# Optimization experiments

Measured on AMD Instinct MI355X. Metric: run time of the kernel, lower is better.

## Reference

```python
import jax, jax.numpy as jnp
import numpy as np

DIM = 1024
NUM_HEADS = 16
HEAD_DIM = DIM // NUM_HEADS
B, L = 2, 2048


def setup_inputs() -> dict:
    key = jax.random.key(0)
    k_x, k_qkv, k_pw, k_pb = jax.random.split(key, 4)
    x = jax.random.normal(k_x, (B, L, DIM), dtype=jnp.float32)
    # nn.Linear(dim, 3*dim, bias=False): weight [3*dim, dim]; y = x @ W.T
    w_qkv = jax.random.normal(k_qkv, (3 * DIM, DIM), dtype=jnp.float32) * (DIM ** -0.5)
    # nn.Linear(dim, dim) with bias
    w_proj = jax.random.normal(k_pw, (DIM, DIM), dtype=jnp.float32) * (DIM ** -0.5)
    b_proj = jax.random.normal(k_pb, (DIM,), dtype=jnp.float32) * 0.01
    return {"x": x, "w_qkv": w_qkv, "w_proj": w_proj, "b_proj": b_proj}


def reference(x, w_qkv, w_proj, b_proj):
    Bx, Lx, C = x.shape
    qkv = x @ w_qkv.T  # [B, L, 3C]
    qkv = qkv.reshape(Bx, Lx, 3, NUM_HEADS, HEAD_DIM)
    q = jnp.transpose(qkv[:, :, 0], (0, 2, 1, 3))  # [B, H, L, D]
    k = jnp.transpose(qkv[:, :, 1], (0, 2, 1, 3))
    v = jnp.transpose(qkv[:, :, 2], (0, 2, 1, 3))
    attn = jnp.einsum('bhqd,bhkd->bhqk', q, k) * (HEAD_DIM ** -0.5)
    attn = jax.nn.softmax(attn, axis=-1)
    out = jnp.einsum('bhqk,bhkd->bhqd', attn, v)  # [B, H, L, D]
    out = jnp.transpose(out, (0, 2, 1, 3)).reshape(Bx, Lx, C)
    return out @ w_proj.T + b_proj
```

## Files before the change

### kernel.cpp

```cpp
#include <hip/hip_runtime.h>

#define DIM 1024
#define NH 16
#define HD 64
#define BB 2
#define LL 2048
#define BL (BB*LL)
#define NQKV (3*DIM)

typedef __bf16 bf16;
typedef __bf16 bf16x4 __attribute__((ext_vector_type(4)));
typedef __bf16 bf16x8 __attribute__((ext_vector_type(8)));
typedef float  f32x4  __attribute__((ext_vector_type(4)));

#define QSCALE 0.1803368801111204f

typedef __attribute__((address_space(3))) unsigned int lds_u32;
typedef __attribute__((address_space(1))) unsigned int glb_u32;

__device__ __forceinline__ void gld_lds16(const bf16* g, bf16* l) {
    __builtin_amdgcn_global_load_lds((const glb_u32*)g, (lds_u32*)l, 16, 0, 0);
}

#define C0 (BL*DIM/4)
#define C1 (NQKV*DIM/4)
#define C2 (DIM*DIM/4)
__global__ __launch_bounds__(256) void cvt_all(const float* __restrict__ x,
        const float* __restrict__ wq, const float* __restrict__ wp,
        bf16* __restrict__ xb, bf16* __restrict__ wqb, bf16* __restrict__ wpb) {
    int i = blockIdx.x * 256 + threadIdx.x;
    const float* in; bf16* out; int j;
    if (i < C0)            { in = x;  out = xb;  j = i; }
    else if (i < C0 + C1)  { in = wq; out = wqb; j = i - C0; }
    else                   { in = wp; out = wpb; j = i - C0 - C1; }
    float4 f = ((const float4*)in)[j];
    bf16x4 o = { (bf16)f.x, (bf16)f.y, (bf16)f.z, (bf16)f.w };
    ((bf16x4*)out)[j] = o;
}

__global__ __launch_bounds__(256, 3) void gemm_qkv(
        const bf16* __restrict__ A, const bf16* __restrict__ W,
        bf16* __restrict__ Qb, bf16* __restrict__ Kb, bf16* __restrict__ VTb) {
    __shared__ bf16 As[128][64];
    __shared__ bf16 Bs[128][64];
    const int tid = threadIdx.x;
    const int w = tid >> 6, lane = tid & 63, quad = lane >> 4, l16 = lane & 15;
    const int n0 = blockIdx.x * 128, m0 = blockIdx.y * 128;
    const int wm = (w & 1) * 64, wn = (w >> 1) * 64;
    f32x4 acc[4][4] = {};
    for (int k0 = 0; k0 < DIM; k0 += 64) {
        #pragma unroll
        for (int i = 0; i < 4; ++i) {
            int cb = w * 256 + i * 64;
            int gc = cb + lane;
            int r = gc >> 3;
            int cs = (gc & 7) ^ (r & 7);
            gld_lds16(A + (size_t)(m0 + r) * DIM + k0 + cs*8, &As[0][0] + cb * 8);
            gld_lds16(W + (size_t)(n0 + r) * DIM + k0 + cs*8, &Bs[0][0] + cb * 8);
        }
        __syncthreads();
        #pragma unroll
        for (int kc = 0; kc < 2; ++kc) {
            bf16x8 af[4], bfr[4];
            #pragma unroll
            for (int t = 0; t < 4; ++t) {
                int rw = wn + t*16 + l16;
                int cw = (kc*4 + quad) ^ (rw & 7);
                af[t] = *(const bf16x8*)(&Bs[0][0] + rw*64 + cw*8);
                int rx = wm + t*16 + l16;
                int cx = (kc*4 + quad) ^ (rx & 7);
                bfr[t] = *(const bf16x8*)(&As[0][0] + rx*64 + cx*8);
            }
            #pragma unroll
            for (int tm = 0; tm < 4; ++tm)
                #pragma unroll
                for (int tn = 0; tn < 4; ++tn)
                    acc[tm][tn] = __builtin_amdgcn_mfma_f32_16x16x32_bf16(
                                      af[tm], bfr[tn], acc[tm][tn], 0, 0, 0);
        }
        __syncthreads();
    }
    const int which = n0 >> 10;
    #pragma unroll
    for (int tm = 0; tm < 4; ++tm) {
        int nb = n0 + wn + tm*16 + quad*4;
        int rem = nb & 1023, h = rem >> 6, db = rem & 63;
        #pragma unroll
        for (int tn = 0; tn < 4; ++tn) {
            int m = m0 + wm + tn*16 + l16;
            int b = m >> 11, l = m & 2047, bh = (b << 4) | h;
            if (which == 0) {
                bf16x4 q4 = { (bf16)(acc[tm][tn][0] * QSCALE),
                              (bf16)(acc[tm][tn][1] * QSCALE),
                              (bf16)(acc[tm][tn][2] * QSCALE),
                              (bf16)(acc[tm][tn][3] * QSCALE) };
                *(bf16x4*)(Qb + ((size_t)bh << 17) + ((size_t)l << 6) + db) = q4;
            } else if (which == 1) {
                bf16x4 k4 = { (bf16)acc[tm][tn][0], (bf16)acc[tm][tn][1],
                              (bf16)acc[tm][tn][2], (bf16)acc[tm][tn][3] };
                *(bf16x4*)(Kb + ((size_t)bh << 17) + ((size_t)l << 6) + db) = k4;
            } else {
                #pragma unroll
                for (int r = 0; r < 4; ++r)
                    VTb[((size_t)bh << 17) + ((size_t)(db + r) << 11) + l] =
                        (bf16)acc[tm][tn][r];
            }
        }
    }
}

__global__ __launch_bounds__(256, 3) void gemm_proj(
        const bf16* __restrict__ A, const bf16* __restrict__ W,
        const float* __restrict__ bias, float* __restrict__ out) {
    __shared__ bf16 As[2][128][64];
    __shared__ bf16 Bs[2][64][64];
    const int tid = threadIdx.x;
    const int w = tid >> 6, lane = tid & 63, quad = lane >> 4, l16 = lane & 15;
    const int n0 = blockIdx.x * 64, m0 = blockIdx.y * 128;
    const int wm = (w & 1) * 64, wn = (w >> 1) * 32;
    f32x4 acc[2][4] = {};

    auto stage = [&](int k0, int buf) {
        #pragma unroll
        for (int i = 0; i < 4; ++i) {
            int cb = w * 256 + i * 64;
            int gc = cb + lane;
            int r = gc >> 3;
            int cs = (gc & 7) ^ (r & 7);
            gld_lds16(A + (size_t)(m0 + r) * DIM + k0 + cs*8,
                      &As[buf][0][0] + cb * 8);
        }
        #pragma unroll
        for (int i = 0; i < 2; ++i) {
            int cb = w * 128 + i * 64;
            int gc = cb + lane;
            int r = gc >> 3;
            int cs = (gc & 7) ^ (r & 7);
            gld_lds16(W + (size_t)(n0 + r) * DIM + k0 + cs*8,
                      &Bs[buf][0][0] + cb * 8);
        }
    };

    stage(0, 0);
    for (int ks = 0; ks < 16; ++ks) {
        const int cur = ks & 1;
        __syncthreads();
        if (ks < 15) stage((ks + 1) * 64, cur ^ 1);
        #pragma unroll
        for (int kc = 0; kc < 2; ++kc) {
            bf16x8 af[2], bfr[4];
            #pragma unroll
            for (int t = 0; t < 2; ++t) {
                int rw = wn + t*16 + l16;
                int cw = (kc*4 + quad) ^ (rw & 7);
                af[t] = *(const bf16x8*)(&Bs[cur][0][0] + rw*64 + cw*8);
            }
            #pragma unroll
            for (int t = 0; t < 4; ++t) {
                int rx = wm + t*16 + l16;
                int cx = (kc*4 + quad) ^ (rx & 7);
                bfr[t] = *(const bf16x8*)(&As[cur][0][0] + rx*64 + cx*8);
            }
            #pragma unroll
            for (int tm = 0; tm < 2; ++tm)
                #pragma unroll
                for (int tn = 0; tn < 4; ++tn)
                    acc[tm][tn] = __builtin_amdgcn_mfma_f32_16x16x32_bf16(
                                      af[tm], bfr[tn], acc[tm][tn], 0, 0, 0);
        }
    }
    #pragma unroll
    for (int tm = 0; tm < 2; ++tm) {
        int nb = n0 + wn + tm*16 + quad*4;
        float4 b4 = *(const float4*)&bias[nb];
        #pragma unroll
        for (int tn = 0; tn < 4; ++tn) {
            int m = m0 + wm + tn*16 + l16;
            float4 o4 = { acc[tm][tn][0] + b4.x, acc[tm][tn][1] + b4.y,
                          acc[tm][tn][2] + b4.z, acc[tm][tn][3] + b4.w };
            *(float4*)(out + (size_t)m * DIM + nb) = o4;
        }
    }
}

__global__ __launch_bounds__(512, 2) void attn(
        const bf16* __restrict__ Qb, const bf16* __restrict__ Kb,
        const bf16* __restrict__ VTb, bf16* __restrict__ AO) {
    __shared__ __align__(16) char smem[66048];
    bf16* KsP  = (bf16*)smem;
    bf16* VTsP = (bf16*)(smem + 32768);
    const int tid = threadIdx.x;
    const int w = tid >> 6, lane = tid & 63, quad = lane >> 4, l16 = lane & 15;
    const int qw = w & 3, kvh = w >> 2;
    const int linear = blockIdx.y * 8 + blockIdx.x;
    const int swz = (linear & 7) * 32 + (linear >> 3);
    const int qt = swz & 7, bh = swz >> 3;
    const bf16* Qg = Qb + ((size_t)bh << 17) + (size_t)(qt * 256) * 64;
    const bf16* Kg = Kb + ((size_t)bh << 17);
    const bf16* Vg = VTb + ((size_t)bh << 17);

    bf16x8 aq[4][2];
    #pragma unroll
    for (int sub = 0; sub < 4; ++sub)
        #pragma unroll
        for (int kd = 0; kd < 2; ++kd)
            aq[sub][kd] = *(const bf16x8*)(Qg + (size_t)(qw*64 + sub*16 + l16) * 64
                                           + kd*32 + quad*8);

    bf16x8 onesf = {};
    if (l16 == 0)
        #pragma unroll
        for (int j = 0; j < 8; ++j) onesf[j] = (bf16)1.0f;

    f32x4 oacc[4][4] = {};
    f32x4 lacc[4] = {};
    const f32x4 zero4 = {};
    bf16x8 ap[4][2];

    auto stageK = [&](int kt, int buf) {
        #pragma unroll
        for (int sub = 0; sub < 2; ++sub) {
            int r = tid >> 3;
            int cs = (tid & 7) ^ (r & 7) ^ ((r >> 3) & 7) ^ ((r & 1) << 2);
            gld_lds16(Kg + (size_t)(kt*128 + sub*64 + r) * 64 + cs*8,
                      KsP + (buf*2 + sub) * 4096 + tid*8);
        }
    };
    auto stageV = [&](int kt, int buf) {
        #pragma unroll
        for (int sub = 0; sub < 2; ++sub) {
            int r = tid >> 3;
            int cs = (tid & 7) ^ (r & 7) ^ ((r >> 3) & 7);
            gld_lds16(Vg + (size_t)r * 2048 + kt*128 + sub*64 + cs*8,
                      VTsP + (buf*2 + sub) * 4096 + tid*8);
        }
    };
    auto pv = [&](int pbuf) {
        __builtin_amdgcn_s_setprio(1);
        #pragma unroll
        for (int kk = 0; kk < 2; ++kk) {
            #pragma unroll
            for (int nt = 0; nt < 4; ++nt) {
                int row = nt*16 + l16;
                int cp = (kk*4 + quad) ^ (row & 7) ^ ((row >> 3) & 7);
                bf16x8 bv = *(const bf16x8*)(VTsP + (pbuf*2 + kvh) * 4096
                                             + row*64 + cp*8);
                #pragma unroll
                for (int sub = 0; sub < 4; ++sub)
                    oacc[sub][nt] = __builtin_amdgcn_mfma_f32_16x16x32_bf16(
                                        ap[sub][kk], bv, oacc[sub][nt], 0, 0, 0);
            }
            #pragma unroll
            for (int sub = 0; sub < 4; ++sub)
                lacc[sub] = __builtin_amdgcn_mfma_f32_16x16x32_bf16(
                                ap[sub][kk], onesf, lacc[sub], 0, 0, 0);
        }
        __builtin_amdgcn_s_setprio(0);
    };

    auto body = [&](int kt, int cur) {
        __syncthreads();
        if (kt < 15) stageK(kt + 1, cur ^ 1);
        stageV(kt, cur);

        if (kt > 0) pv(cur ^ 1);

        f32x4 s[4][2][2];
        __builtin_amdgcn_s_setprio(1);
        #pragma unroll
        for (int kk = 0; kk < 2; ++kk)
            #pragma unroll
            for (int u = 0; u < 2; ++u) {
                int rk = kk*32 + ((l16 >> 2) << 3) + u*4 + (l16 & 3);
                int f = (rk & 7) ^ ((rk >> 3) & 7) ^ ((rk & 1) << 2);
                const bf16* kb = KsP + (cur*2 + kvh) * 4096 + rk*64;
                bf16x8 kf0 = *(const bf16x8*)(kb + ((0*4 + quad) ^ f)*8);
                bf16x8 kf1 = *(const bf16x8*)(kb + ((1*4 + quad) ^ f)*8);
                #pragma unroll
                for (int sub = 0; sub < 4; ++sub) {
                    s[sub][kk][u] = __builtin_amdgcn_mfma_f32_16x16x32_bf16(
                                        kf0, aq[sub][0], zero4, 0, 0, 0);
                    s[sub][kk][u] = __builtin_amdgcn_mfma_f32_16x16x32_bf16(
                                        kf1, aq[sub][1], s[sub][kk][u], 0, 0, 0);
                }
            }
        __builtin_amdgcn_s_setprio(0);

        #pragma unroll
        for (int sub = 0; sub < 4; ++sub)
            #pragma unroll
            for (int kk = 0; kk < 2; ++kk) {
                bf16x8 p;
                #pragma unroll
                for (int u = 0; u < 2; ++u)
                    #pragma unroll
                    for (int r = 0; r < 4; ++r)
                        p[u*4 + r] = (bf16)__builtin_amdgcn_exp2f(s[sub][kk][u][r]);
                ap[sub][kk] = p;
            }
    };

    stageK(0, 0);
    for (int kt2 = 0; kt2 < 16; kt2 += 2) {
        body(kt2,     0);
        body(kt2 + 1, 1);
    }
    __syncthreads();
    pv(1);

    float* OredF = (float*)smem;
    float* LredF = (float*)(smem + 32768);
    const int b = bh >> 4, h = bh & 15;
    #pragma unroll
    for (int t = 0; t < 2; ++t) {
        __syncthreads();
        if (kvh == 1 && (qw >> 1) == t) {
            int slot = qw & 1;
            #pragma unroll
            for (int sub = 0; sub < 4; ++sub)
                #pragma unroll
                for (int nt = 0; nt < 4; ++nt)
                    #pragma unroll
                    for (int r = 0; r < 4; ++r)
                        OredF[((slot*4 + sub)*16 + quad*4 + r)*64 + nt*16 + l16]
                            = oacc[sub][nt][r];
            if (l16 == 0)
                #pragma unroll
                for (int sub = 0; sub < 4; ++sub)
                    #pragma unroll
                    for (int r = 0; r < 4; ++r)
                        LredF[(slot*4 + sub)*16 + quad*4 + r] = lacc[sub][r];
        }
        __syncthreads();
        if (kvh == 0 && (qw >> 1) == t) {
            int slot = qw & 1;
            #pragma unroll
            for (int sub = 0; sub < 4; ++sub)
                #pragma unroll
                for (int nt = 0; nt < 4; ++nt)
                    #pragma unroll
                    for (int r = 0; r < 4; ++r)
                        oacc[sub][nt][r] +=
                            OredF[((slot*4 + sub)*16 + quad*4 + r)*64 + nt*16 + l16];
            if (l16 == 0)
                #pragma unroll
                for (int sub = 0; sub < 4; ++sub)
                    #pragma unroll
                    for (int r = 0; r < 4; ++r)
                        lacc[sub][r] += LredF[(slot*4 + sub)*16 + quad*4 + r];
            #pragma unroll
            for (int sub = 0; sub < 4; ++sub)
                #pragma unroll
                for (int r = 0; r < 4; ++r) {
                    float l = __shfl(lacc[sub][r], quad * 16, 64);
                    float inv = 1.0f / l;
                    int lq = qt*256 + qw*64 + sub*16 + quad*4 + r;
                    size_t rowbase = ((size_t)(b * 2048 + lq)) * DIM + h * 64;
                    #pragma unroll
                    for (int nt = 0; nt < 4; ++nt)
                        AO[rowbase + nt*16 + l16] = (bf16)(oacc[sub][nt][r] * inv);
                }
        }
    }
}

extern "C" void kernel_launch(void* const* d_in, const int* in_sizes, int n_in,
                              void* d_out, int out_size, void* d_ws, size_t ws_size,
                              hipStream_t stream) {
    const float* x      = (const float*)d_in[0];
    const float* w_qkv  = (const float*)d_in[1];
    const float* w_proj = (const float*)d_in[2];
    const float* b_proj = (const float*)d_in[3];
    float* out = (float*)d_out;
    char* ws = (char*)d_ws;

    bf16* xb  = (bf16*)(ws);
    bf16* wqb = (bf16*)(ws + ( 8u << 20));
    bf16* wpb = (bf16*)(ws + (14u << 20));
    bf16* Qb  = (bf16*)(ws + (16u << 20));
    bf16* Kb  = (bf16*)(ws + (24u << 20));
    bf16* VTb = (bf16*)(ws + (32u << 20));
    bf16* AOb = (bf16*)(ws + (40u << 20));

    cvt_all<<<(C0 + C1 + C2) / 256, 256, 0, stream>>>(x, w_qkv, w_proj, xb, wqb, wpb);
    gemm_qkv<<<dim3(NQKV/128, BL/128), 256, 0, stream>>>(xb, wqb, Qb, Kb, VTb);
    attn<<<dim3(LL/256, BB*NH),        512, 0, stream>>>(Qb, Kb, VTb, AOb);
    gemm_proj<<<dim3(DIM/64, BL/128),  256, 0, stream>>>(AOb, wpb, b_proj, out);
}
```

Measured before the change: 166.5 us.

## Enlarge proj GEMM tile to 128x128 and drop double buffering

```diff
diff --git a/kernel.cpp b/kernel.cpp
--- a/kernel.cpp
+++ b/kernel.cpp
@@ -112,65 +112,47 @@
 __global__ __launch_bounds__(256, 3) void gemm_proj(
         const bf16* __restrict__ A, const bf16* __restrict__ W,
         const float* __restrict__ bias, float* __restrict__ out) {
-    __shared__ bf16 As[2][128][64];
-    __shared__ bf16 Bs[2][64][64];
+    __shared__ bf16 As[128][64];
+    __shared__ bf16 Bs[128][64];
     const int tid = threadIdx.x;
     const int w = tid >> 6, lane = tid & 63, quad = lane >> 4, l16 = lane & 15;
-    const int n0 = blockIdx.x * 64, m0 = blockIdx.y * 128;
-    const int wm = (w & 1) * 64, wn = (w >> 1) * 32;
-    f32x4 acc[2][4] = {};
-
-    auto stage = [&](int k0, int buf) {
+    const int n0 = blockIdx.x * 128, m0 = blockIdx.y * 128;
+    const int wm = (w & 1) * 64, wn = (w >> 1) * 64;
+    f32x4 acc[4][4] = {};
+    for (int k0 = 0; k0 < DIM; k0 += 64) {
         #pragma unroll
         for (int i = 0; i < 4; ++i) {
             int cb = w * 256 + i * 64;
             int gc = cb + lane;
             int r = gc >> 3;
             int cs = (gc & 7) ^ (r & 7);
-            gld_lds16(A + (size_t)(m0 + r) * DIM + k0 + cs*8,
-                      &As[buf][0][0] + cb * 8);
-        }
-        #pragma unroll
-        for (int i = 0; i < 2; ++i) {
-            int cb = w * 128 + i * 64;
-            int gc = cb + lane;
-            int r = gc >> 3;
-            int cs = (gc & 7) ^ (r & 7);
-            gld_lds16(W + (size_t)(n0 + r) * DIM + k0 + cs*8,
-                      &Bs[buf][0][0] + cb * 8);
-        }
-    };
-
-    stage(0, 0);
-    for (int ks = 0; ks < 16; ++ks) {
-        const int cur = ks & 1;
-        __syncthreads();
-        if (ks < 15) stage((ks + 1) * 64, cur ^ 1);
+            gld_lds16(A + (size_t)(m0 + r) * DIM + k0 + cs*8, &As[0][0] + cb * 8);
+            gld_lds16(W + (size_t)(n0 + r) * DIM + k0 + cs*8, &Bs[0][0] + cb * 8);
+        }
+        __syncthreads();
         #pragma unroll
         for (int kc = 0; kc < 2; ++kc) {
-            bf16x8 af[2], bfr[4];
-            #pragma unroll
-            for (int t = 0; t < 2; ++t) {
+            bf16x8 af[4], bfr[4];
+            #pragma unroll
+            for (int t = 0; t < 4; ++t) {
                 int rw = wn + t*16 + l16;
                 int cw = (kc*4 + quad) ^ (rw & 7);
-                af[t] = *(const bf16x8*)(&Bs[cur][0][0] + rw*64 + cw*8);
-            }
-            #pragma unroll
-            for (int t = 0; t < 4; ++t) {
+                af[t] = *(const bf16x8*)(&Bs[0][0] + rw*64 + cw*8);
                 int rx = wm + t*16 + l16;
                 int cx = (kc*4 + quad) ^ (rx & 7);
-                bfr[t] = *(const bf16x8*)(&As[cur][0][0] + rx*64 + cx*8);
-            }
-            #pragma unroll
-            for (int tm = 0; tm < 2; ++tm)
+                bfr[t] = *(const bf16x8*)(&As[0][0] + rx*64 + cx*8);
+            }
+            #pragma unroll
+            for (int tm = 0; tm < 4; ++tm)
                 #pragma unroll
                 for (int tn = 0; tn < 4; ++tn)
                     acc[tm][tn] = __builtin_amdgcn_mfma_f32_16x16x32_bf16(
                                       af[tm], bfr[tn], acc[tm][tn], 0, 0, 0);
         }
+        __syncthreads();
     }
     #pragma unroll
-    for (int tm = 0; tm < 2; ++tm) {
+    for (int tm = 0; tm < 4; ++tm) {
         int nb = n0 + wn + tm*16 + quad*4;
         float4 b4 = *(const float4*)&bias[nb];
         #pragma unroll
@@ -385,5 +367,5 @@
     cvt_all<<<(C0 + C1 + C2) / 256, 256, 0, stream>>>(x, w_qkv, w_proj, xb, wqb, wpb);
     gemm_qkv<<<dim3(NQKV/128, BL/128), 256, 0, stream>>>(xb, wqb, Qb, Kb, VTb);
     attn<<<dim3(LL/256, BB*NH),        512, 0, stream>>>(Qb, Kb, VTb, AOb);
-    gemm_proj<<<dim3(DIM/64, BL/128),  256, 0, stream>>>(AOb, wpb, b_proj, out);
-}
+    gemm_proj<<<dim3(DIM/128, BL/128), 256, 0, stream>>>(AOb, wpb, b_proj, out);
+}
```

After: 176.4 us. 1.06x slower.

## Split attention KV tile across four wave groups with 1024-thread blocks

Applied to the files above, without the earlier changes.

```diff
diff --git a/kernel.cpp b/kernel.cpp
--- a/kernel.cpp
+++ b/kernel.cpp
@@ -183,10 +183,10 @@
     }
 }
 
-__global__ __launch_bounds__(512, 2) void attn(
+__global__ __launch_bounds__(1024, 4) void attn(
         const bf16* __restrict__ Qb, const bf16* __restrict__ Kb,
         const bf16* __restrict__ VTb, bf16* __restrict__ AO) {
-    __shared__ __align__(16) char smem[66048];
+    __shared__ __align__(16) char smem[66560];
     bf16* KsP  = (bf16*)smem;
     bf16* VTsP = (bf16*)(smem + 32768);
     const int tid = threadIdx.x;
@@ -215,46 +215,39 @@
     f32x4 oacc[4][4] = {};
     f32x4 lacc[4] = {};
     const f32x4 zero4 = {};
-    bf16x8 ap[4][2];
+    bf16x8 ap[4];
 
     auto stageK = [&](int kt, int buf) {
-        #pragma unroll
-        for (int sub = 0; sub < 2; ++sub) {
-            int r = tid >> 3;
-            int cs = (tid & 7) ^ (r & 7) ^ ((r >> 3) & 7) ^ ((r & 1) << 2);
-            gld_lds16(Kg + (size_t)(kt*128 + sub*64 + r) * 64 + cs*8,
-                      KsP + (buf*2 + sub) * 4096 + tid*8);
-        }
+        int sub = tid >> 9, tl = tid & 511;
+        int r = tl >> 3;
+        int cs = (tl & 7) ^ (r & 7) ^ ((r >> 3) & 7) ^ ((r & 1) << 2);
+        gld_lds16(Kg + (size_t)(kt*128 + sub*64 + r) * 64 + cs*8,
+                  KsP + (buf*2 + sub) * 4096 + tl*8);
     };
     auto stageV = [&](int kt, int buf) {
-        #pragma unroll
-        for (int sub = 0; sub < 2; ++sub) {
-            int r = tid >> 3;
-            int cs = (tid & 7) ^ (r & 7) ^ ((r >> 3) & 7);
-            gld_lds16(Vg + (size_t)r * 2048 + kt*128 + sub*64 + cs*8,
-                      VTsP + (buf*2 + sub) * 4096 + tid*8);
-        }
+        int sub = tid >> 9, tl = tid & 511;
+        int r = tl >> 3;
+        int cs = (tl & 7) ^ (r & 7) ^ ((r >> 3) & 7);
+        gld_lds16(Vg + (size_t)r * 2048 + kt*128 + sub*64 + cs*8,
+                  VTsP + (buf*2 + sub) * 4096 + tl*8);
     };
     auto pv = [&](int pbuf) {
         __builtin_amdgcn_s_setprio(1);
         #pragma unroll
-        for (int kk = 0; kk < 2; ++kk) {
-            #pragma unroll
-            for (int nt = 0; nt < 4; ++nt) {
-                int row = nt*16 + l16;
-                int cp = (kk*4 + quad) ^ (row & 7) ^ ((row >> 3) & 7);
-                bf16x8 bv = *(const bf16x8*)(VTsP + (pbuf*2 + kvh) * 4096
-                                             + row*64 + cp*8);
-                #pragma unroll
-                for (int sub = 0; sub < 4; ++sub)
-                    oacc[sub][nt] = __builtin_amdgcn_mfma_f32_16x16x32_bf16(
-                                        ap[sub][kk], bv, oacc[sub][nt], 0, 0, 0);
-            }
-            #pragma unroll
-            for (int sub = 0; sub < 4; ++sub)
-                lacc[sub] = __builtin_amdgcn_mfma_f32_16x16x32_bf16(
-                                ap[sub][kk], onesf, lacc[sub], 0, 0, 0);
-        }
+        for (int nt = 0; nt < 4; ++nt) {
+            int row = nt*16 + l16;
+            int cp = ((kvh & 1)*4 + quad) ^ (row & 7) ^ ((row >> 3) & 7);
+            bf16x8 bv = *(const bf16x8*)(VTsP + (pbuf*2 + (kvh >> 1)) * 4096
+                                         + row*64 + cp*8);
+            #pragma unroll
+            for (int sub = 0; sub < 4; ++sub)
+                oacc[sub][nt] = __builtin_amdgcn_mfma_f32_16x16x32_bf16(
+                                    ap[sub], bv, oacc[sub][nt], 0, 0, 0);
+        }
+        #pragma unroll
+        for (int sub = 0; sub < 4; ++sub)
+            lacc[sub] = __builtin_amdgcn_mfma_f32_16x16x32_bf16(
+                            ap[sub], onesf, lacc[sub], 0, 0, 0);
         __builtin_amdgcn_s_setprio(0);
     };
 
@@ -265,39 +258,35 @@
 
         if (kt > 0) pv(cur ^ 1);
 
-        f32x4 s[4][2][2];
+        f32x4 s[4][2];
         __builtin_amdgcn_s_setprio(1);
         #pragma unroll
-        for (int kk = 0; kk < 2; ++kk)
-            #pragma unroll
-            for (int u = 0; u < 2; ++u) {
-                int rk = kk*32 + ((l16 >> 2) << 3) + u*4 + (l16 & 3);
-                int f = (rk & 7) ^ ((rk >> 3) & 7) ^ ((rk & 1) << 2);
-                const bf16* kb = KsP + (cur*2 + kvh) * 4096 + rk*64;
-                bf16x8 kf0 = *(const bf16x8*)(kb + ((0*4 + quad) ^ f)*8);
-                bf16x8 kf1 = *(const bf16x8*)(kb + ((1*4 + quad) ^ f)*8);
-                #pragma unroll
-                for (int sub = 0; sub < 4; ++sub) {
-                    s[sub][kk][u] = __builtin_amdgcn_mfma_f32_16x16x32_bf16(
-                                        kf0, aq[sub][0], zero4, 0, 0, 0);
-                    s[sub][kk][u] = __builtin_amdgcn_mfma_f32_16x16x32_bf16(
-                                        kf1, aq[sub][1], s[sub][kk][u], 0, 0, 0);
-                }
+        for (int u = 0; u < 2; ++u) {
+            int rk = (kvh & 1)*32 + ((l16 >> 2) << 3) + u*4 + (l16 & 3);
+            int f = (rk & 7) ^ ((rk >> 3) & 7) ^ ((rk & 1) << 2);
+            const bf16* kb = KsP + (cur*2 + (kvh >> 1)) * 4096 + rk*64;
+            bf16x8 kf0 = *(const bf16x8*)(kb + ((0*4 + quad) ^ f)*8);
+            bf16x8 kf1 = *(const bf16x8*)(kb + ((1*4 + quad) ^ f)*8);
+            #pragma unroll
+            for (int sub = 0; sub < 4; ++sub) {
+                s[sub][u] = __builtin_amdgcn_mfma_f32_16x16x32_bf16(
+                                kf0, aq[sub][0], zero4, 0, 0, 0);
+                s[sub][u] = __builtin_amdgcn_mfma_f32_16x16x32_bf16(
+                                kf1, aq[sub][1], s[sub][u], 0, 0, 0);
             }
+        }
         __builtin_amdgcn_s_setprio(0);
 
         #pragma unroll
-        for (int sub = 0; sub < 4; ++sub)
-            #pragma unroll
-            for (int kk = 0; kk < 2; ++kk) {
-                bf16x8 p;
-                #pragma unroll
-                for (int u = 0; u < 2; ++u)
-                    #pragma unroll
-                    for (int r = 0; r < 4; ++r)
-                        p[u*4 + r] = (bf16)__builtin_amdgcn_exp2f(s[sub][kk][u][r]);
-                ap[sub][kk] = p;
-            }
+        for (int sub = 0; sub < 4; ++sub) {
+            bf16x8 p;
+            #pragma unroll
+            for (int u = 0; u < 2; ++u)
+                #pragma unroll
+                for (int r = 0; r < 4; ++r)
+                    p[u*4 + r] = (bf16)__builtin_amdgcn_exp2f(s[sub][u][r]);
+            ap[sub] = p;
+        }
     };
 
     stageK(0, 0);
@@ -309,13 +298,14 @@
     pv(1);
 
     float* OredF = (float*)smem;
-    float* LredF = (float*)(smem + 32768);
+    float* LredF = (float*)(smem + 65536);
     const int b = bh >> 4, h = bh & 15;
     #pragma unroll
     for (int t = 0; t < 2; ++t) {
-        __syncthreads();
-        if (kvh == 1 && (qw >> 1) == t) {
-            int slot = qw & 1;
+        const bool grp = (qw >> 1) == t;
+        __syncthreads();
+        if (grp && (kvh & 1)) {
+            int slot = (qw & 1)*2 + (kvh >> 1);
             #pragma unroll
             for (int sub = 0; sub < 4; ++sub)
                 #pragma unroll
@@ -332,8 +322,44 @@
                         LredF[(slot*4 + sub)*16 + quad*4 + r] = lacc[sub][r];
         }
         __syncthreads();
-        if (kvh == 0 && (qw >> 1) == t) {
-            int slot = qw & 1;
+        if (grp && !(kvh & 1)) {
+            int slot = (qw & 1)*2 + (kvh >> 1);
+            #pragma unroll
+            for (int sub = 0; sub < 4; ++sub)
+                #pragma unroll
+                for (int nt = 0; nt < 4; ++nt)
+                    #pragma unroll
+                    for (int r = 0; r < 4; ++r)
+                        oacc[sub][nt][r] +=
+                            OredF[((slot*4 + sub)*16 + quad*4 + r)*64 + nt*16 + l16];
+            if (l16 == 0)
+                #pragma unroll
+                for (int sub = 0; sub < 4; ++sub)
+                    #pragma unroll
+                    for (int r = 0; r < 4; ++r)
+                        lacc[sub][r] += LredF[(slot*4 + sub)*16 + quad*4 + r];
+        }
+        __syncthreads();
+        if (grp && kvh == 2) {
+            int slot = (qw & 1)*2;
+            #pragma unroll
+            for (int sub = 0; sub < 4; ++sub)
+                #pragma unroll
+                for (int nt = 0; nt < 4; ++nt)
+                    #pragma unroll
+                    for (int r = 0; r < 4; ++r)
+                        OredF[((slot*4 + sub)*16 + quad*4 + r)*64 + nt*16 + l16]
+                            = oacc[sub][nt][r];
+            if (l16 == 0)
+                #pragma unroll
+                for (int sub = 0; sub < 4; ++sub)
+                    #pragma unroll
+                    for (int r = 0; r < 4; ++r)
+                        LredF[(slot*4 + sub)*16 + quad*4 + r] = lacc[sub][r];
+        }
+        __syncthreads();
+        if (grp && kvh == 0) {
+            int slot = (qw & 1)*2;
             #pragma unroll
             for (int sub = 0; sub < 4; ++sub)
                 #pragma unroll
@@ -384,6 +410,6 @@
 
     cvt_all<<<(C0 + C1 + C2) / 256, 256, 0, stream>>>(x, w_qkv, w_proj, xb, wqb, wpb);
     gemm_qkv<<<dim3(NQKV/128, BL/128), 256, 0, stream>>>(xb, wqb, Qb, Kb, VTb);
-    attn<<<dim3(LL/256, BB*NH),        512, 0, stream>>>(Qb, Kb, VTb, AOb);
+    attn<<<dim3(LL/256, BB*NH),        1024, 0, stream>>>(Qb, Kb, VTb, AOb);
     gemm_proj<<<dim3(DIM/64, BL/128),  256, 0, stream>>>(AOb, wpb, b_proj, out);
 }
```

After: 457.6 us. 175% more time.
